# Kernel tuning notes

Hardware: AMD Instinct MI355X
Metric: run time of the kernel (lower is better)

Reference implementation:

```python
import jax, jax.numpy as jnp
import numpy as np

MUL0, MUL1, SCALARS_OUT = 16, 16, 128
L0, L1 = MUL0, MUL1 * 3            # 16, 48
PATH_NUMEL = MUL0 * MUL1 * SCALARS_OUT  # 32768 per path, two paths
EPS = 1e-5
# e3nn normalization: irrep_normalization='component' -> alpha = dim(ir_out) = 1;
# path_normalization='element' -> divide by sum over paths to same output of mul1*mul2 = 256+256 = 512.
PATH_COEFF = 1.0 / np.sqrt(512.0)
CG_110 = 1.0 / np.sqrt(3.0)  # wigner_3j(1,1,0)[i,j] = delta_ij/sqrt(3) (unit Frobenius norm)


def layer_norm(x, g, b):
    mu = jnp.mean(x, axis=-1, keepdims=True)
    var = jnp.mean(jnp.square(x - mu), axis=-1, keepdims=True)
    return (x - mu) * jax.lax.rsqrt(var + EPS) * g + b


def ff_block(x, g, b, w1, w2, b2):
    # LayerNorm -> Linear(no bias) -> SiLU -> Linear(bias); residual=False in both uses
    h = jax.nn.silu(layer_norm(x, g, b) @ w1)
    return h @ w2 + b2


def setup_inputs() -> dict:
    key = jax.random.key(0)
    ks = jax.random.split(key, 8)
    N = 2048
    return {
        "x": jax.random.normal(ks[0], (N, L0 + L1), dtype=jnp.float32),
        "we_ln_g": jnp.ones((L0,), jnp.float32),
        "we_ln_b": jnp.zeros((L0,), jnp.float32),
        "we_w1": jax.random.normal(ks[1], (L0, 4 * L0), jnp.float32) / np.sqrt(L0),
        "we_w2": jax.random.normal(ks[2], (4 * L0, 2 * PATH_NUMEL), jnp.float32) / np.sqrt(4 * L0),
        "we_b2": jnp.zeros((2 * PATH_NUMEL,), jnp.float32),
        "om_ln_g": jnp.ones((SCALARS_OUT,), jnp.float32),
        "om_ln_b": jnp.zeros((SCALARS_OUT,), jnp.float32),
        "om_w1": jax.random.normal(ks[3], (SCALARS_OUT, 4 * SCALARS_OUT), jnp.float32) / np.sqrt(SCALARS_OUT),
        "om_w2": jax.random.normal(ks[4], (4 * SCALARS_OUT, 1), jnp.float32) / np.sqrt(4 * SCALARS_OUT),
        "om_b2": jnp.zeros((1,), jnp.float32),
    }


def reference(x, we_ln_g, we_ln_b, we_w1, we_w2, we_b2,
              om_ln_g, om_ln_b, om_w1, om_w2, om_b2):
    N = x.shape[0]
    feats = x[:, :L0]                       # [N, 16] scalars (0e)
    x1 = x[:, L0:].reshape(N, MUL1, 3)      # [N, 16, 3] vectors (1o)

    # per-sample tensor-product weights (shared_weights=False)
    w = ff_block(feats, we_ln_g, we_ln_b, we_w1, we_w2, we_b2)  # [N, 65536]
    w0 = w[:, :PATH_NUMEL].reshape(N, MUL0, MUL0, SCALARS_OUT)
    w1 = w[:, PATH_NUMEL:].reshape(N, MUL1, MUL1, SCALARS_OUT)

    # path 0: 0e x 0e -> 0e  (uvw)
    o0 = jnp.einsum('nu,nv,nuvw->nw', feats, feats, w0)
    # path 1: 1o x 1o -> 0e  (uvw, CG = delta_ij/sqrt(3))
    o1 = jnp.einsum('nui,nvi,nuvw->nw', x1, x1, w1) * CG_110
    tp_out = PATH_COEFF * (o0 + o1)          # [N, 128]

    return ff_block(tp_out, om_ln_g, om_ln_b, om_w1, om_w2, om_b2)  # [N, 1]
```

## Files before the change

kernel.cpp:

```cpp
#include <hip/hip_runtime.h>
#include <hip/hip_bf16.h>
#include <cstdint>

#define EPS 1e-5f
#define PATH_COEFF 0.04419417382415922f
#define CG110     0.5773502691896258f

typedef __bf16 v8bf __attribute__((ext_vector_type(8)));
typedef float  v4f  __attribute__((ext_vector_type(4)));

static __device__ __forceinline__ unsigned short f2bf(float x){
    unsigned int u = __builtin_bit_cast(unsigned int, x);
    u += 0x7fffu + ((u >> 16) & 1u);
    return (unsigned short)(u >> 16);
}
static __device__ __forceinline__ unsigned short f2h(float x){
    return __builtin_bit_cast(unsigned short, (_Float16)x);
}
static __device__ __forceinline__ float h2f(unsigned short b){
    return (float)__builtin_bit_cast(_Float16, b);
}

__global__ __launch_bounds__(256)
void k_convV(const float* __restrict__ w2, const float* __restrict__ b2,
             unsigned short* __restrict__ Vt2)
{
    __shared__ unsigned short tile[32][128];
    int k    = blockIdx.x / 4;
    int slab = blockIdx.x & 3;
    int t    = threadIdx.x;
    const float* srcbase = (k < 64) ? (w2 + (size_t)k * 65536) : b2;

    for (int chunk = 0; chunk < 4; ++chunk){
        int pbase = slab*128 + chunk*32;
        #pragma unroll
        for (int i = 0; i < 4; ++i){
            int g = t + 256*i;
            int ploc = g >> 5, c4 = g & 31;
            const float4 v = *(const float4*)(srcbase + (size_t)(pbase + ploc)*128 + c4*4);
            unsigned int w0 = (unsigned)f2bf(v.x) | ((unsigned)f2bf(v.y) << 16);
            unsigned int w1 = (unsigned)f2bf(v.z) | ((unsigned)f2bf(v.w) << 16);
            *(uint2*)&tile[ploc][c4*4] = make_uint2(w0, w1);
        }
        __syncthreads();
        int w = t & 127, h = t >> 7;
        int ps = slab*4 + chunk;
        unsigned int words[8];
        #pragma unroll
        for (int g2 = 0; g2 < 8; ++g2)
            words[g2] = (unsigned)tile[h*16 + g2*2][w] | ((unsigned)tile[h*16 + g2*2 + 1][w] << 16);
        unsigned short* dq0 = Vt2 + (((size_t)(k*16 + ps)*4 + 2*h    )*128 + w)*8;
        unsigned short* dq1 = Vt2 + (((size_t)(k*16 + ps)*4 + 2*h + 1)*128 + w)*8;
        *(uint4*)dq0 = make_uint4(words[0], words[1], words[2], words[3]);
        *(uint4*)dq1 = make_uint4(words[4], words[5], words[6], words[7]);
        __syncthreads();
    }
}

__global__ __launch_bounds__(256)
void k_convW(const float* __restrict__ w1, unsigned short* __restrict__ w1t)
{
    __shared__ unsigned short tile[32][128];
    int j0 = blockIdx.x * 128;
    int t  = threadIdx.x;
    for (int chunk = 0; chunk < 4; ++chunk){
        #pragma unroll
        for (int i = 0; i < 4; ++i){
            int g = t + 256*i;
            int wloc = g >> 5, c4 = g & 31;
            int w = chunk*32 + wloc;
            const float4 v = *(const float4*)(w1 + (size_t)w*512 + j0 + c4*4);
            unsigned int a = (unsigned)f2bf(v.x) | ((unsigned)f2bf(v.y) << 16);
            unsigned int b = (unsigned)f2bf(v.z) | ((unsigned)f2bf(v.w) << 16);
            *(uint2*)&tile[wloc][c4*4] = make_uint2(a, b);
        }
        __syncthreads();
        int jl = t & 127, h = t >> 7;
        unsigned int words[8];
        #pragma unroll
        for (int g2 = 0; g2 < 8; ++g2)
            words[g2] = (unsigned)tile[h*16 + g2*2][jl] | ((unsigned)tile[h*16 + g2*2 + 1][jl] << 16);
        unsigned short* dst = w1t + (size_t)(j0 + jl)*128 + chunk*32 + h*16;
        *(uint4*)dst       = make_uint4(words[0], words[1], words[2], words[3]);
        *(uint4*)(dst + 8) = make_uint4(words[4], words[5], words[6], words[7]);
        __syncthreads();
    }
}

__global__ __launch_bounds__(64)
void k_prep(const float* __restrict__ x, const float* __restrict__ lng,
            const float* __restrict__ lnb, const float* __restrict__ w1,
            unsigned short* __restrict__ Q2, float* __restrict__ Ht, int N)
{
    int row  = blockIdx.x;
    int lane = threadIdx.x;
    const float* xr = x + (size_t)row * 64;
    float f[16]; float mu = 0.f;
    #pragma unroll
    for (int u = 0; u < 16; ++u){ f[u] = xr[u]; mu += f[u]; }
    mu *= (1.f/16.f);
    float var = 0.f;
    #pragma unroll
    for (int u = 0; u < 16; ++u){ float d = f[u] - mu; var += d*d; }
    var *= (1.f/16.f);
    float inv = rsqrtf(var + EPS);
    float lnf[16];
    #pragma unroll
    for (int u = 0; u < 16; ++u) lnf[u] = (f[u]-mu)*inv*lng[u] + lnb[u];
    float h1 = 0.f;
    #pragma unroll
    for (int u = 0; u < 16; ++u) h1 += lnf[u] * w1[u*64 + lane];
    float h = h1 / (1.f + expf(-h1));
    Ht[(size_t)lane * N + row] = h;
    if (lane == 0) Ht[(size_t)64 * N + row] = 1.f;

    union { unsigned short qs[8]; uint4 v; } qu;
    #pragma unroll
    for (int j = 0; j < 8; ++j){
        int p = lane*8 + j;
        float q;
        if (p < 256){
            int u = p >> 4, v = p & 15;
            q = PATH_COEFF * f[u] * f[v];
        } else {
            int pp = p - 256;
            int u = pp >> 4, v = pp & 15;
            const float* ya = xr + 16 + u*3;
            const float* yb = xr + 16 + v*3;
            q = (PATH_COEFF * CG110) * (ya[0]*yb[0] + ya[1]*yb[1] + ya[2]*yb[2]);
        }
        qu.qs[j] = f2bf(q);
    }
    int rb = row >> 6, r64 = row & 63;
    int ps = lane >> 2, quad = lane & 3;
    *(uint4*)(Q2 + (((size_t)(rb*16 + ps)*4 + quad)*64 + r64)*8) = qu.v;
}

__global__ __launch_bounds__(256, 4)
void k_main(const unsigned short* __restrict__ Q2, const unsigned short* __restrict__ Vt2,
            const float* __restrict__ Ht, unsigned short* __restrict__ partial, int N)
{
    int tid  = threadIdx.x;
    int lane = tid & 63, wv = tid >> 6;
    int r2 = wv >> 1, c2 = wv & 1;
    int quad = lane >> 4, l16 = lane & 15;
    int mb = blockIdx.x / 65, kb = blockIdx.x % 65;
    int rowbase = mb*128 + r2*64;
    int rb = rowbase >> 6;
    int wbase = c2*64;

    const unsigned short* aroot = Q2  + (size_t)rb*32768 + quad*512  + l16*8;
    const unsigned short* broot = Vt2 + (size_t)kb*65536 + quad*1024 + (wbase + l16)*8;

    v4f acc[4][4];
    #pragma unroll
    for (int m=0;m<4;++m)
      #pragma unroll
      for (int n=0;n<4;++n)
        #pragma unroll
        for (int r=0;r<4;++r) acc[m][n][r] = 0.f;

    #pragma unroll 4
    for (int ps = 0; ps < 16; ++ps){
        const unsigned short* ap = aroot + ps*2048;
        const unsigned short* bp = broot + ps*4096;
        v8bf a[4], bb[4];
        #pragma unroll
        for (int m=0;m<4;++m) a[m]  = *(const v8bf*)(ap + m*128);
        #pragma unroll
        for (int n=0;n<4;++n) bb[n] = *(const v8bf*)(bp + n*128);
        #pragma unroll
        for (int m=0;m<4;++m)
          #pragma unroll
          for (int n=0;n<4;++n)
            acc[m][n] = __builtin_amdgcn_mfma_f32_16x16x32_bf16(a[m], bb[n], acc[m][n], 0, 0, 0);
    }

    const float* hp = Ht + (size_t)kb*N + rowbase + quad*4;
    unsigned short* pp = partial + (size_t)kb*N*128 + ((size_t)rowbase + quad*4)*128 + wbase + l16;
    #pragma unroll
    for (int m=0;m<4;++m){
        v4f hv = *(const v4f*)(hp + m*16);
        #pragma unroll
        for (int n=0;n<4;++n)
          #pragma unroll
          for (int r=0;r<4;++r)
            pp[(size_t)(m*16 + r)*128 + n*16] = f2h(hv[r]*acc[m][n][r]);
    }
}

__global__ __launch_bounds__(128)
void k_red(const unsigned short* __restrict__ partial, const float* __restrict__ g,
           const float* __restrict__ b, unsigned short* __restrict__ lnf, int N)
{
    int row = blockIdx.x, t = threadIdx.x;
    const unsigned short* p0 = partial + (size_t)row*128 + t;
    float s = 0.f;
    #pragma unroll
    for (int sl = 0; sl < 65; ++sl) s += h2f(p0[(size_t)sl*N*128]);
    float a = s, q = s*s;
    #pragma unroll
    for (int off = 32; off > 0; off >>= 1){
        a += __shfl_down(a, off, 64);
        q += __shfl_down(q, off, 64);
    }
    __shared__ float red[4];
    int wv = t >> 6;
    if ((t & 63) == 0){ red[wv*2] = a; red[wv*2+1] = q; }
    __syncthreads();
    float sum = red[0] + red[2], sumsq = red[1] + red[3];
    float mu  = sum * (1.f/128.f);
    float var = sumsq * (1.f/128.f) - mu*mu;
    float inv = rsqrtf(var + EPS);
    lnf[(size_t)row*128 + t] = f2bf((s - mu)*inv*g[t] + b[t]);
}

__global__ __launch_bounds__(128)
void k_mlp2(const unsigned short* __restrict__ lnf, const unsigned short* __restrict__ w1t,
            const float* __restrict__ w2, const float* __restrict__ b2,
            float* __restrict__ out, int N)
{
    int tid = threadIdx.x, lane = tid & 63, wv = tid >> 6;
    int quad = lane >> 4, l16 = lane & 15;
    int MB = N >> 6;
    int mb = blockIdx.x % MB, jb = blockIdx.x / MB;
    int rowbase = mb*64, jbase = jb*128 + wv*64;

    v4f acc[4][4];
    #pragma unroll
    for (int m=0;m<4;++m)
      #pragma unroll
      for (int n=0;n<4;++n)
        #pragma unroll
        for (int r=0;r<4;++r) acc[m][n][r] = 0.f;

    #pragma unroll
    for (int ps = 0; ps < 4; ++ps){
        v8bf a[4], bb[4];
        #pragma unroll
        for (int m=0;m<4;++m)
            a[m]  = *(const v8bf*)(lnf + (size_t)(rowbase + m*16 + l16)*128 + ps*32 + quad*8);
        #pragma unroll
        for (int n=0;n<4;++n)
            bb[n] = *(const v8bf*)(w1t + (size_t)(jbase + n*16 + l16)*128 + ps*32 + quad*8);
        #pragma unroll
        for (int m=0;m<4;++m)
          #pragma unroll
          for (int n=0;n<4;++n)
            acc[m][n] = __builtin_amdgcn_mfma_f32_16x16x32_bf16(a[m], bb[n], acc[m][n], 0, 0, 0);
    }

    float w2v[4];
    #pragma unroll
    for (int n=0;n<4;++n) w2v[n] = w2[jbase + n*16 + l16];

    bool first = (jb == 0) && (wv == 0);
    #pragma unroll
    for (int m=0;m<4;++m){
        #pragma unroll
        for (int r=0;r<4;++r){
            float ssum = 0.f;
            #pragma unroll
            for (int n=0;n<4;++n){
                float v = acc[m][n][r];
                ssum += (v / (1.f + expf(-v))) * w2v[n];
            }
            #pragma unroll
            for (int off=8; off>0; off>>=1) ssum += __shfl_xor(ssum, off, 64);
            if (l16 == 0){
                float add = ssum + (first ? b2[0] : 0.f);
                atomicAdd(&out[rowbase + m*16 + quad*4 + r], add);
            }
        }
    }
}

extern "C" void kernel_launch(void* const* d_in, const int* in_sizes, int n_in,
                              void* d_out, int out_size, void* d_ws, size_t ws_size,
                              hipStream_t stream)
{
    const float* x     = (const float*)d_in[0];
    const float* we_g  = (const float*)d_in[1];
    const float* we_b  = (const float*)d_in[2];
    const float* we_w1 = (const float*)d_in[3];
    const float* we_w2 = (const float*)d_in[4];
    const float* we_b2 = (const float*)d_in[5];
    const float* om_g  = (const float*)d_in[6];
    const float* om_b  = (const float*)d_in[7];
    const float* om_w1 = (const float*)d_in[8];
    const float* om_w2 = (const float*)d_in[9];
    const float* om_b2 = (const float*)d_in[10];

    int N  = in_sizes[0] / 64;

    char* ws = (char*)d_ws;
    size_t offV = 0;
    size_t szV  = (size_t)65*16*4*128*8*2;
    size_t offQ = offV + szV;
    size_t szQ  = (size_t)N*512*2;
    size_t offH = offQ + szQ;
    size_t szH  = (size_t)65*N*4;
    size_t offP = offH + szH;
    size_t szP  = (size_t)65*N*128*2;
    size_t offL = offP + szP;
    size_t szL  = (size_t)N*128*2;
    size_t offW = offL + szL;

    unsigned short* Vt2 = (unsigned short*)(ws + offV);
    unsigned short* Q2  = (unsigned short*)(ws + offQ);
    float* Ht           = (float*)(ws + offH);
    unsigned short* Par = (unsigned short*)(ws + offP);
    unsigned short* Lnf = (unsigned short*)(ws + offL);
    unsigned short* W1t = (unsigned short*)(ws + offW);
    float* out = (float*)d_out;

    hipMemsetAsync(d_out, 0, (size_t)N*4, stream);
    hipLaunchKernelGGL(k_convV, dim3(65*4),      dim3(256), 0, stream, we_w2, we_b2, Vt2);
    hipLaunchKernelGGL(k_convW, dim3(4),         dim3(256), 0, stream, om_w1, W1t);
    hipLaunchKernelGGL(k_prep,  dim3(N),         dim3(64),  0, stream, x, we_g, we_b, we_w1, Q2, Ht, N);
    hipLaunchKernelGGL(k_main,  dim3((N/128)*65),dim3(256), 0, stream, Q2, Vt2, Ht, Par, N);
    hipLaunchKernelGGL(k_red,   dim3(N),         dim3(128), 0, stream, Par, om_g, om_b, Lnf, N);
    hipLaunchKernelGGL(k_mlp2,  dim3((N/64)*4),  dim3(128), 0, stream, Lnf, W1t, om_w2, om_b2, out, N);
}
```

Before: 150.4 us.

## Merge prep kernels, pair k-slabs in main GEMM, drop atomics in final MLP

Fuses the weight conversion, om_w1 transpose and per-row prep into one launch, with prep reworked to one row per thread through swizzled shared memory. The main kernel now handles two hidden units per block and sums them before writing, which halves the fp16 partial buffer and the reduction reads. The final MLP uses a single block per 64 rows that reduces in shared memory, replacing the memset and atomics. In exchange the main kernel carries double the accumulators under reduced occupancy bounds, the hard-coded 272 blocks assumes N=2048, and prep does more serial work per thread.

```diff
diff --git a/kernel.cpp b/kernel.cpp
--- a/kernel.cpp
+++ b/kernel.cpp
@@ -22,121 +22,134 @@
 }
 
 __global__ __launch_bounds__(256)
-void k_convV(const float* __restrict__ w2, const float* __restrict__ b2,
-             unsigned short* __restrict__ Vt2)
-{
-    __shared__ unsigned short tile[32][128];
-    int k    = blockIdx.x / 4;
-    int slab = blockIdx.x & 3;
-    int t    = threadIdx.x;
-    const float* srcbase = (k < 64) ? (w2 + (size_t)k * 65536) : b2;
-
-    for (int chunk = 0; chunk < 4; ++chunk){
-        int pbase = slab*128 + chunk*32;
-        #pragma unroll
-        for (int i = 0; i < 4; ++i){
-            int g = t + 256*i;
-            int ploc = g >> 5, c4 = g & 31;
-            const float4 v = *(const float4*)(srcbase + (size_t)(pbase + ploc)*128 + c4*4);
-            unsigned int w0 = (unsigned)f2bf(v.x) | ((unsigned)f2bf(v.y) << 16);
-            unsigned int w1 = (unsigned)f2bf(v.z) | ((unsigned)f2bf(v.w) << 16);
-            *(uint2*)&tile[ploc][c4*4] = make_uint2(w0, w1);
-        }
+void k_mega(const float* __restrict__ w2, const float* __restrict__ b2,
+            unsigned short* __restrict__ Vt2,
+            const float* __restrict__ om_w1, unsigned short* __restrict__ w1t,
+            const float* __restrict__ x, const float* __restrict__ lng,
+            const float* __restrict__ lnb, const float* __restrict__ we_w1,
+            unsigned short* __restrict__ Q2, float* __restrict__ Ht, int N)
+{
+    __shared__ __align__(16) char smem[65536];
+    int b = blockIdx.x;
+    int t = threadIdx.x;
+
+    if (b < 260){
+        unsigned short (*tile)[128] = (unsigned short (*)[128])smem;
+        int k    = b >> 2;
+        int slab = b & 3;
+        const float* srcbase = (k < 64) ? (w2 + (size_t)k * 65536) : b2;
+        for (int chunk = 0; chunk < 4; ++chunk){
+            int pbase = slab*128 + chunk*32;
+            #pragma unroll
+            for (int i = 0; i < 4; ++i){
+                int g = t + 256*i;
+                int ploc = g >> 5, c4 = g & 31;
+                const float4 v = *(const float4*)(srcbase + (size_t)(pbase + ploc)*128 + c4*4);
+                unsigned int w0 = (unsigned)f2bf(v.x) | ((unsigned)f2bf(v.y) << 16);
+                unsigned int w1 = (unsigned)f2bf(v.z) | ((unsigned)f2bf(v.w) << 16);
+                *(uint2*)&tile[ploc][c4*4] = make_uint2(w0, w1);
+            }
+            __syncthreads();
+            int w = t & 127, h = t >> 7;
+            int ps = slab*4 + chunk;
+            unsigned int words[8];
+            #pragma unroll
+            for (int g2 = 0; g2 < 8; ++g2)
+                words[g2] = (unsigned)tile[h*16 + g2*2][w] | ((unsigned)tile[h*16 + g2*2 + 1][w] << 16);
+            unsigned short* dq0 = Vt2 + (((size_t)(k*16 + ps)*4 + 2*h    )*128 + w)*8;
+            unsigned short* dq1 = Vt2 + (((size_t)(k*16 + ps)*4 + 2*h + 1)*128 + w)*8;
+            *(uint4*)dq0 = make_uint4(words[0], words[1], words[2], words[3]);
+            *(uint4*)dq1 = make_uint4(words[4], words[5], words[6], words[7]);
+            __syncthreads();
+        }
+    } else if (b < 264){
+        unsigned short (*tile)[128] = (unsigned short (*)[128])smem;
+        int j0 = (b - 260) * 128;
+        for (int chunk = 0; chunk < 4; ++chunk){
+            #pragma unroll
+            for (int i = 0; i < 4; ++i){
+                int g = t + 256*i;
+                int wloc = g >> 5, c4 = g & 31;
+                int w = chunk*32 + wloc;
+                const float4 v = *(const float4*)(om_w1 + (size_t)w*512 + j0 + c4*4);
+                unsigned int a = (unsigned)f2bf(v.x) | ((unsigned)f2bf(v.y) << 16);
+                unsigned int bb = (unsigned)f2bf(v.z) | ((unsigned)f2bf(v.w) << 16);
+                *(uint2*)&tile[wloc][c4*4] = make_uint2(a, bb);
+            }
+            __syncthreads();
+            int jl = t & 127, h = t >> 7;
+            unsigned int words[8];
+            #pragma unroll
+            for (int g2 = 0; g2 < 8; ++g2)
+                words[g2] = (unsigned)tile[h*16 + g2*2][jl] | ((unsigned)tile[h*16 + g2*2 + 1][jl] << 16);
+            unsigned short* dst = w1t + (size_t)(j0 + jl)*128 + chunk*32 + h*16;
+            *(uint4*)dst       = make_uint4(words[0], words[1], words[2], words[3]);
+            *(uint4*)(dst + 8) = make_uint4(words[4], words[5], words[6], words[7]);
+            __syncthreads();
+        }
+    } else {
+        float* xs = (float*)smem;
+        int wv = t >> 6, lane = t & 63;
+        int rbase = (b - 264)*256 + wv*64;
+        for (int i = 0; i < 64; ++i)
+            xs[wv*4096 + i*64 + (lane ^ (i & 31))] = x[(size_t)(rbase + i)*64 + lane];
         __syncthreads();
-        int w = t & 127, h = t >> 7;
-        int ps = slab*4 + chunk;
-        unsigned int words[8];
-        #pragma unroll
-        for (int g2 = 0; g2 < 8; ++g2)
-            words[g2] = (unsigned)tile[h*16 + g2*2][w] | ((unsigned)tile[h*16 + g2*2 + 1][w] << 16);
-        unsigned short* dq0 = Vt2 + (((size_t)(k*16 + ps)*4 + 2*h    )*128 + w)*8;
-        unsigned short* dq1 = Vt2 + (((size_t)(k*16 + ps)*4 + 2*h + 1)*128 + w)*8;
-        *(uint4*)dq0 = make_uint4(words[0], words[1], words[2], words[3]);
-        *(uint4*)dq1 = make_uint4(words[4], words[5], words[6], words[7]);
-        __syncthreads();
-    }
-}
-
-__global__ __launch_bounds__(256)
-void k_convW(const float* __restrict__ w1, unsigned short* __restrict__ w1t)
-{
-    __shared__ unsigned short tile[32][128];
-    int j0 = blockIdx.x * 128;
-    int t  = threadIdx.x;
-    for (int chunk = 0; chunk < 4; ++chunk){
-        #pragma unroll
-        for (int i = 0; i < 4; ++i){
-            int g = t + 256*i;
-            int wloc = g >> 5, c4 = g & 31;
-            int w = chunk*32 + wloc;
-            const float4 v = *(const float4*)(w1 + (size_t)w*512 + j0 + c4*4);
-            unsigned int a = (unsigned)f2bf(v.x) | ((unsigned)f2bf(v.y) << 16);
-            unsigned int b = (unsigned)f2bf(v.z) | ((unsigned)f2bf(v.w) << 16);
-            *(uint2*)&tile[wloc][c4*4] = make_uint2(a, b);
-        }
-        __syncthreads();
-        int jl = t & 127, h = t >> 7;
-        unsigned int words[8];
-        #pragma unroll
-        for (int g2 = 0; g2 < 8; ++g2)
-            words[g2] = (unsigned)tile[h*16 + g2*2][jl] | ((unsigned)tile[h*16 + g2*2 + 1][jl] << 16);
-        unsigned short* dst = w1t + (size_t)(j0 + jl)*128 + chunk*32 + h*16;
-        *(uint4*)dst       = make_uint4(words[0], words[1], words[2], words[3]);
-        *(uint4*)(dst + 8) = make_uint4(words[4], words[5], words[6], words[7]);
-        __syncthreads();
-    }
-}
-
-__global__ __launch_bounds__(64)
-void k_prep(const float* __restrict__ x, const float* __restrict__ lng,
-            const float* __restrict__ lnb, const float* __restrict__ w1,
-            unsigned short* __restrict__ Q2, float* __restrict__ Ht, int N)
-{
-    int row  = blockIdx.x;
-    int lane = threadIdx.x;
-    const float* xr = x + (size_t)row * 64;
-    float f[16]; float mu = 0.f;
-    #pragma unroll
-    for (int u = 0; u < 16; ++u){ f[u] = xr[u]; mu += f[u]; }
-    mu *= (1.f/16.f);
-    float var = 0.f;
-    #pragma unroll
-    for (int u = 0; u < 16; ++u){ float d = f[u] - mu; var += d*d; }
-    var *= (1.f/16.f);
-    float inv = rsqrtf(var + EPS);
-    float lnf[16];
-    #pragma unroll
-    for (int u = 0; u < 16; ++u) lnf[u] = (f[u]-mu)*inv*lng[u] + lnb[u];
-    float h1 = 0.f;
-    #pragma unroll
-    for (int u = 0; u < 16; ++u) h1 += lnf[u] * w1[u*64 + lane];
-    float h = h1 / (1.f + expf(-h1));
-    Ht[(size_t)lane * N + row] = h;
-    if (lane == 0) Ht[(size_t)64 * N + row] = 1.f;
-
-    union { unsigned short qs[8]; uint4 v; } qu;
-    #pragma unroll
-    for (int j = 0; j < 8; ++j){
-        int p = lane*8 + j;
-        float q;
-        if (p < 256){
-            int u = p >> 4, v = p & 15;
-            q = PATH_COEFF * f[u] * f[v];
-        } else {
-            int pp = p - 256;
-            int u = pp >> 4, v = pp & 15;
-            const float* ya = xr + 16 + u*3;
-            const float* yb = xr + 16 + v*3;
-            q = (PATH_COEFF * CG110) * (ya[0]*yb[0] + ya[1]*yb[1] + ya[2]*yb[2]);
-        }
-        qu.qs[j] = f2bf(q);
-    }
-    int rb = row >> 6, r64 = row & 63;
-    int ps = lane >> 2, quad = lane & 3;
-    *(uint4*)(Q2 + (((size_t)(rb*16 + ps)*4 + quad)*64 + r64)*8) = qu.v;
-}
-
-__global__ __launch_bounds__(256, 4)
+        int row = rbase + lane;
+        float xr[64];
+        #pragma unroll
+        for (int c = 0; c < 64; ++c)
+            xr[c] = xs[wv*4096 + lane*64 + (c ^ (lane & 31))];
+
+        float mu = 0.f;
+        #pragma unroll
+        for (int u = 0; u < 16; ++u) mu += xr[u];
+        mu *= (1.f/16.f);
+        float var = 0.f;
+        #pragma unroll
+        for (int u = 0; u < 16; ++u){ float d = xr[u]-mu; var += d*d; }
+        var *= (1.f/16.f);
+        float inv = rsqrtf(var + EPS);
+        float lnf[16];
+        #pragma unroll
+        for (int u = 0; u < 16; ++u) lnf[u] = (xr[u]-mu)*inv*lng[u] + lnb[u];
+
+        for (int k = 0; k < 64; ++k){
+            float hk = 0.f;
+            #pragma unroll
+            for (int u = 0; u < 16; ++u) hk += lnf[u] * we_w1[u*64 + k];
+            hk = hk / (1.f + expf(-hk));
+            Ht[(size_t)k*N + row] = hk;
+        }
+        Ht[(size_t)64*N + row] = 1.f;
+
+        int rb = rbase >> 6;
+        #pragma unroll
+        for (int ps = 0; ps < 16; ++ps){
+            #pragma unroll
+            for (int quad = 0; quad < 4; ++quad){
+                union { unsigned short qs[8]; uint4 v; } qu;
+                #pragma unroll
+                for (int j = 0; j < 8; ++j){
+                    int p = ps*32 + quad*8 + j;
+                    float q;
+                    if (p < 256){
+                        int u = p >> 4, v = p & 15;
+                        q = PATH_COEFF * xr[u] * xr[v];
+                    } else {
+                        int pp = p - 256;
+                        int u = pp >> 4, v = pp & 15;
+                        q = (PATH_COEFF * CG110) * (xr[16+u*3]*xr[16+v*3]
+                           + xr[17+u*3]*xr[17+v*3] + xr[18+u*3]*xr[18+v*3]);
+                    }
+                    qu.qs[j] = f2bf(q);
+                }
+                *(uint4*)(Q2 + (((size_t)(rb*16 + ps)*4 + quad)*64 + lane)*8) = qu.v;
+            }
+        }
+    }
+}
+
+__global__ __launch_bounds__(256, 2)
 void k_main(const unsigned short* __restrict__ Q2, const unsigned short* __restrict__ Vt2,
             const float* __restrict__ Ht, unsigned short* __restrict__ partial, int N)
 {
@@ -144,48 +157,68 @@
     int lane = tid & 63, wv = tid >> 6;
     int r2 = wv >> 1, c2 = wv & 1;
     int quad = lane >> 4, l16 = lane & 15;
-    int mb = blockIdx.x / 65, kb = blockIdx.x % 65;
+    int mb = blockIdx.x / 33, c = blockIdx.x % 33;
+    int k0 = c*2;
+    bool two = (c < 32);
     int rowbase = mb*128 + r2*64;
     int rb = rowbase >> 6;
     int wbase = c2*64;
 
     const unsigned short* aroot = Q2  + (size_t)rb*32768 + quad*512  + l16*8;
-    const unsigned short* broot = Vt2 + (size_t)kb*65536 + quad*1024 + (wbase + l16)*8;
-
-    v4f acc[4][4];
+    const unsigned short* b0r   = Vt2 + (size_t)k0*65536 + quad*1024 + (wbase + l16)*8;
+    const unsigned short* b1r   = b0r + 65536;
+
+    v4f t0[4][4], t1[4][4];
     #pragma unroll
     for (int m=0;m<4;++m)
       #pragma unroll
       for (int n=0;n<4;++n)
         #pragma unroll
-        for (int r=0;r<4;++r) acc[m][n][r] = 0.f;
+        for (int r=0;r<4;++r){ t0[m][n][r] = 0.f; t1[m][n][r] = 0.f; }
 
     #pragma unroll 4
     for (int ps = 0; ps < 16; ++ps){
         const unsigned short* ap = aroot + ps*2048;
-        const unsigned short* bp = broot + ps*4096;
-        v8bf a[4], bb[4];
-        #pragma unroll
-        for (int m=0;m<4;++m) a[m]  = *(const v8bf*)(ap + m*128);
-        #pragma unroll
-        for (int n=0;n<4;++n) bb[n] = *(const v8bf*)(bp + n*128);
-        #pragma unroll
-        for (int m=0;m<4;++m)
-          #pragma unroll
-          for (int n=0;n<4;++n)
-            acc[m][n] = __builtin_amdgcn_mfma_f32_16x16x32_bf16(a[m], bb[n], acc[m][n], 0, 0, 0);
-    }
-
-    const float* hp = Ht + (size_t)kb*N + rowbase + quad*4;
-    unsigned short* pp = partial + (size_t)kb*N*128 + ((size_t)rowbase + quad*4)*128 + wbase + l16;
+        v8bf a[4];
+        #pragma unroll
+        for (int m=0;m<4;++m) a[m] = *(const v8bf*)(ap + m*128);
+        {
+            const unsigned short* bp = b0r + ps*4096;
+            v8bf bb[4];
+            #pragma unroll
+            for (int n=0;n<4;++n) bb[n] = *(const v8bf*)(bp + n*128);
+            #pragma unroll
+            for (int m=0;m<4;++m)
+              #pragma unroll
+              for (int n=0;n<4;++n)
+                t0[m][n] = __builtin_amdgcn_mfma_f32_16x16x32_bf16(a[m], bb[n], t0[m][n], 0, 0, 0);
+        }
+        if (two){
+            const unsigned short* bp = b1r + ps*4096;
+            v8bf bb[4];
+            #pragma unroll
+            for (int n=0;n<4;++n) bb[n] = *(const v8bf*)(bp + n*128);
+            #pragma unroll
+            for (int m=0;m<4;++m)
+              #pragma unroll
+              for (int n=0;n<4;++n)
+                t1[m][n] = __builtin_amdgcn_mfma_f32_16x16x32_bf16(a[m], bb[n], t1[m][n], 0, 0, 0);
+        }
+    }
+
+    const float* hp0 = Ht + (size_t)k0*N + rowbase + quad*4;
+    unsigned short* pp = partial + (size_t)c*N*128 + ((size_t)rowbase + quad*4)*128 + wbase + l16;
     #pragma unroll
     for (int m=0;m<4;++m){
-        v4f hv = *(const v4f*)(hp + m*16);
+        v4f hv0 = *(const v4f*)(hp0 + m*16);
+        v4f hv1;
+        if (two) hv1 = *(const v4f*)(hp0 + N + m*16);
+        else { hv1[0]=hv1[1]=hv1[2]=hv1[3]=0.f; }
         #pragma unroll
         for (int n=0;n<4;++n)
           #pragma unroll
           for (int r=0;r<4;++r)
-            pp[(size_t)(m*16 + r)*128 + n*16] = f2h(hv[r]*acc[m][n][r]);
+            pp[(size_t)(m*16 + r)*128 + n*16] = f2h(hv0[r]*t0[m][n][r] + hv1[r]*t1[m][n][r]);
     }
 }
 
@@ -197,7 +230,7 @@
     const unsigned short* p0 = partial + (size_t)row*128 + t;
     float s = 0.f;
     #pragma unroll
-    for (int sl = 0; sl < 65; ++sl) s += h2f(p0[(size_t)sl*N*128]);
+    for (int sl = 0; sl < 33; ++sl) s += h2f(p0[(size_t)sl*N*128]);
     float a = s, q = s*s;
     #pragma unroll
     for (int off = 32; off > 0; off >>= 1){
@@ -215,64 +248,63 @@
     lnf[(size_t)row*128 + t] = f2bf((s - mu)*inv*g[t] + b[t]);
 }
 
-__global__ __launch_bounds__(128)
+__global__ __launch_bounds__(256)
 void k_mlp2(const unsigned short* __restrict__ lnf, const unsigned short* __restrict__ w1t,
             const float* __restrict__ w2, const float* __restrict__ b2,
             float* __restrict__ out, int N)
 {
+    __shared__ float red2[4][64];
     int tid = threadIdx.x, lane = tid & 63, wv = tid >> 6;
     int quad = lane >> 4, l16 = lane & 15;
-    int MB = N >> 6;
-    int mb = blockIdx.x % MB, jb = blockIdx.x / MB;
-    int rowbase = mb*64, jbase = jb*128 + wv*64;
-
-    v4f acc[4][4];
+    int rowbase = blockIdx.x * 64;
+    int jbase = wv * 128;
+
+    v4f acc[4][8];
     #pragma unroll
     for (int m=0;m<4;++m)
       #pragma unroll
-      for (int n=0;n<4;++n)
+      for (int n=0;n<8;++n)
         #pragma unroll
         for (int r=0;r<4;++r) acc[m][n][r] = 0.f;
 
     #pragma unroll
     for (int ps = 0; ps < 4; ++ps){
-        v8bf a[4], bb[4];
+        v8bf a[4], bb[8];
         #pragma unroll
         for (int m=0;m<4;++m)
             a[m]  = *(const v8bf*)(lnf + (size_t)(rowbase + m*16 + l16)*128 + ps*32 + quad*8);
         #pragma unroll
-        for (int n=0;n<4;++n)
+        for (int n=0;n<8;++n)
             bb[n] = *(const v8bf*)(w1t + (size_t)(jbase + n*16 + l16)*128 + ps*32 + quad*8);
         #pragma unroll
         for (int m=0;m<4;++m)
           #pragma unroll
-          for (int n=0;n<4;++n)
+          for (int n=0;n<8;++n)
             acc[m][n] = __builtin_amdgcn_mfma_f32_16x16x32_bf16(a[m], bb[n], acc[m][n], 0, 0, 0);
     }
 
-    float w2v[4];
-    #pragma unroll
-    for (int n=0;n<4;++n) w2v[n] = w2[jbase + n*16 + l16];
-
-    bool first = (jb == 0) && (wv == 0);
+    float w2v[8];
+    #pragma unroll
+    for (int n=0;n<8;++n) w2v[n] = w2[jbase + n*16 + l16];
+
     #pragma unroll
     for (int m=0;m<4;++m){
         #pragma unroll
         for (int r=0;r<4;++r){
-            float ssum = 0.f;
-            #pragma unroll
-            for (int n=0;n<4;++n){
+            float s = 0.f;
+            #pragma unroll
+            for (int n=0;n<8;++n){
                 float v = acc[m][n][r];
-                ssum += (v / (1.f + expf(-v))) * w2v[n];
+                s += (v / (1.f + expf(-v))) * w2v[n];
             }
             #pragma unroll
-            for (int off=8; off>0; off>>=1) ssum += __shfl_xor(ssum, off, 64);
-            if (l16 == 0){
-                float add = ssum + (first ? b2[0] : 0.f);
-                atomicAdd(&out[rowbase + m*16 + quad*4 + r], add);
-            }
-        }
-    }
+            for (int off=8; off>0; off>>=1) s += __shfl_xor(s, off, 16);
+            if (l16 == 0) red2[wv][m*16 + quad*4 + r] = s;
+        }
+    }
+    __syncthreads();
+    if (tid < 64)
+        out[rowbase + tid] = red2[0][tid] + red2[1][tid] + red2[2][tid] + red2[3][tid] + b2[0];
 }
 
 extern "C" void kernel_launch(void* const* d_in, const int* in_sizes, int n_in,
@@ -301,7 +333,7 @@
     size_t offH = offQ + szQ;
     size_t szH  = (size_t)65*N*4;
     size_t offP = offH + szH;
-    size_t szP  = (size_t)65*N*128*2;
+    size_t szP  = (size_t)33*N*128*2;
     size_t offL = offP + szP;
     size_t szL  = (size_t)N*128*2;
     size_t offW = offL + szL;
@@ -314,11 +346,9 @@
     unsigned short* W1t = (unsigned short*)(ws + offW);
     float* out = (float*)d_out;
 
-    hipMemsetAsync(d_out, 0, (size_t)N*4, stream);
-    hipLaunchKernelGGL(k_convV, dim3(65*4),      dim3(256), 0, stream, we_w2, we_b2, Vt2);
-    hipLaunchKernelGGL(k_convW, dim3(4),         dim3(256), 0, stream, om_w1, W1t);
-    hipLaunchKernelGGL(k_prep,  dim3(N),         dim3(64),  0, stream, x, we_g, we_b, we_w1, Q2, Ht, N);
-    hipLaunchKernelGGL(k_main,  dim3((N/128)*65),dim3(256), 0, stream, Q2, Vt2, Ht, Par, N);
-    hipLaunchKernelGGL(k_red,   dim3(N),         dim3(128), 0, stream, Par, om_g, om_b, Lnf, N);
-    hipLaunchKernelGGL(k_mlp2,  dim3((N/64)*4),  dim3(128), 0, stream, Lnf, W1t, om_w2, om_b2, out, N);
-}
+    hipLaunchKernelGGL(k_mega, dim3(272),       dim3(256), 0, stream,
+                       we_w2, we_b2, Vt2, om_w1, W1t, x, we_g, we_b, we_w1, Q2, Ht, N);
+    hipLaunchKernelGGL(k_main, dim3(16*33),     dim3(256), 0, stream, Q2, Vt2, Ht, Par, N);
+    hipLaunchKernelGGL(k_red,  dim3(N),         dim3(128), 0, stream, Par, om_g, om_b, Lnf, N);
+    hipLaunchKernelGGL(k_mlp2, dim3(N/64),      dim3(256), 0, stream, Lnf, W1t, om_w2, om_b2, out, N);
+}
```

Result: slower. 163.2 us (+8.6%).
